# Optimization experiments

Hardware: AMD Instinct MI355X
Metric: run time of the kernel (lower is better)

Reference implementation:

```python
import jax, jax.numpy as jnp
import numpy as np

B, S, T = 512, 1024, 48  # batch, seq_len, num_tags


def setup_inputs() -> dict:
    key = jax.random.key(0)
    k1, k2, k3, k4, k5, k6 = jax.random.split(key, 6)
    emissions = jax.random.normal(k1, (B, S, T), dtype=jnp.float32)
    tags = jax.random.randint(k2, (B, S), 0, T)
    lengths = jax.random.randint(k3, (B,), 1, S + 1)
    mask = jnp.arange(S)[None, :] < lengths[:, None]  # contiguous prefix mask, bool
    # learned parameters (nn.Parameter zeros init in the module; use small random here)
    start_transitions = 0.01 * jax.random.normal(k4, (T,), dtype=jnp.float32)
    end_transitions = 0.01 * jax.random.normal(k5, (T,), dtype=jnp.float32)
    transitions = 0.01 * jax.random.normal(k6, (T, T), dtype=jnp.float32)
    return {
        "emissions": emissions,
        "tags": tags,
        "mask": mask,
        "start_transitions": start_transitions,
        "end_transitions": end_transitions,
        "transitions": transitions,
    }


def _log_partition(emissions, mask, start_transitions, end_transitions, transitions):
    # score[b, i] = log-sum over paths ending in tag i (note: this repo indexes
    # transitions[i, j] with j = previous tag inside the partition recursion).
    score0 = start_transitions[None, :] + emissions[:, 0]  # (B, T)

    def step(score, xs):
        emit_t, mask_t = xs  # (B, T), (B,)
        # score_t[b, i] = logsumexp_j(score[b, j] + transitions[i, j]) + emit_t[b, i]
        score_t = jax.nn.logsumexp(score[:, None, :] + transitions[None, :, :], axis=2) + emit_t
        score = jnp.where(mask_t[:, None], score_t, score)
        return score, None

    em = jnp.swapaxes(emissions[:, 1:], 0, 1)  # (S-1, B, T)
    mk = jnp.swapaxes(mask[:, 1:], 0, 1)       # (S-1, B)
    score, _ = jax.lax.scan(step, score0, (em, mk))
    return jax.nn.logsumexp(score + end_transitions[None, :], axis=1)  # (B,)


def _score_sentence(emissions, tags, mask, start_transitions, end_transitions, transitions):
    Bb = emissions.shape[0]
    bidx = jnp.arange(Bb)
    maskf = mask.astype(emissions.dtype)
    score = start_transitions[tags[:, 0]] + emissions[bidx, 0, tags[:, 0]]  # (B,)
    trans_sc = transitions[tags[:, :-1], tags[:, 1:]]  # (B, S-1)
    emit_sc = jnp.take_along_axis(emissions, tags[:, :, None], axis=2)[..., 0]  # (B, S)
    score = score + jnp.sum((trans_sc + emit_sc[:, 1:]) * maskf[:, 1:], axis=1)
    last_idx = jnp.sum(mask.astype(jnp.int32), axis=1) - 1  # (B,)
    last_tags = jnp.take_along_axis(tags, last_idx[:, None], axis=1)[:, 0]
    return score + end_transitions[last_tags]


def reference(emissions, tags, mask, start_transitions, end_transitions, transitions):
    log_denominator = _log_partition(emissions, mask, start_transitions, end_transitions, transitions)
    log_numerator = _score_sentence(emissions, tags, mask, start_transitions, end_transitions, transitions)
    return jnp.mean(log_denominator - log_numerator)
```

## Files before the change

kernel.cpp:

```cpp
#include <hip/hip_runtime.h>

#define BB 512
#define SS 1024
#define TT 48
#define GG 16
#define CK 8
#define NSLOT 5

typedef __attribute__((ext_vector_type(8))) short short8;
typedef __attribute__((ext_vector_type(4))) float float4v;
typedef unsigned uint2v __attribute__((ext_vector_type(2)));

__device__ __forceinline__ unsigned short f2bf(float x) {
    unsigned u = __float_as_uint(x);
    u += 0x7FFFu + ((u >> 16) & 1u);
    return (unsigned short)(u >> 16);
}
__device__ __forceinline__ unsigned pk2bf(float lo, float hi) {
#if __has_builtin(__builtin_amdgcn_cvt_pk_bf16_f32)
    typedef __bf16 bf16x2 __attribute__((ext_vector_type(2)));
    union { bf16x2 v; unsigned u; } cv;
    cv.v = __builtin_amdgcn_cvt_pk_bf16_f32(lo, hi);
    return cv.u;
#else
    return __builtin_amdgcn_perm(__float_as_uint(hi) + 0x8000u,
                                 __float_as_uint(lo) + 0x8000u, 0x07060302u);
#endif
}
__device__ __forceinline__ float bflo(unsigned u) { return __uint_as_float(u << 16); }
__device__ __forceinline__ float bfhi(unsigned u) { return __uint_as_float(u & 0xFFFF0000u); }
__device__ __forceinline__ float wave_sum(float v) {
#pragma unroll
    for (int off = 32; off >= 1; off >>= 1) v += __shfl_xor(v, off, 64);
    return v;
}
__device__ __forceinline__ int wave_sum_i(int v) {
#pragma unroll
    for (int off = 32; off >= 1; off >>= 1) v += __shfl_xor(v, off, 64);
    return v;
}
__device__ __forceinline__ float xgrp_max(float m) {
#if __has_builtin(__builtin_amdgcn_permlane16_swap) && __has_builtin(__builtin_amdgcn_permlane32_swap)
    uint2v a = __builtin_amdgcn_permlane16_swap(__float_as_uint(m), __float_as_uint(m), false, false);
    m = fmaxf(__uint_as_float(a[0]), __uint_as_float(a[1]));
    uint2v b = __builtin_amdgcn_permlane32_swap(__float_as_uint(m), __float_as_uint(m), false, false);
    m = fmaxf(__uint_as_float(b[0]), __uint_as_float(b[1]));
#else
    m = fmaxf(m, __shfl_xor(m, 16, 64));
    m = fmaxf(m, __shfl_xor(m, 32, 64));
#endif
    return m;
}
__device__ __forceinline__ float xgrp_sum(float m) {
#if __has_builtin(__builtin_amdgcn_permlane16_swap) && __has_builtin(__builtin_amdgcn_permlane32_swap)
    uint2v a = __builtin_amdgcn_permlane16_swap(__float_as_uint(m), __float_as_uint(m), false, false);
    m = __uint_as_float(a[0]) + __uint_as_float(a[1]);
    uint2v b = __builtin_amdgcn_permlane32_swap(__float_as_uint(m), __float_as_uint(m), false, false);
    m = __uint_as_float(b[0]) + __uint_as_float(b[1]);
#else
    m += __shfl_xor(m, 16, 64);
    m += __shfl_xor(m, 32, 64);
#endif
    return m;
}

__global__ __launch_bounds__(256)
void crf_numer(const float* __restrict__ em, const int* __restrict__ tags,
               const int* __restrict__ mask, const float* __restrict__ start_tr,
               const float* __restrict__ end_tr, const float* __restrict__ trans,
               float* __restrict__ numer, int* __restrict__ lenArr) {
    const int b = blockIdx.x, tid = threadIdx.x;
    const float* emb = em + (size_t)b * SS * TT;
    const int* tg = tags + (size_t)b * SS;
    const int* mk = mask + (size_t)b * SS;
    const int s0 = tid * 4;
    const int4 t4 = *(const int4*)(tg + s0);
    const int4 m4 = *(const int4*)(mk + s0);
    const int tprev = (tid == 0) ? 0 : tg[s0 - 1];
    int cnt = (m4.x != 0) + (m4.y != 0) + (m4.z != 0) + (m4.w != 0);
    float ns = 0.f;
    if (tid > 0 && m4.x) ns += trans[tprev * TT + t4.x] + emb[(size_t)s0 * TT + t4.x];
    if (m4.y) ns += trans[t4.x * TT + t4.y] + emb[(size_t)(s0 + 1) * TT + t4.y];
    if (m4.z) ns += trans[t4.y * TT + t4.z] + emb[(size_t)(s0 + 2) * TT + t4.z];
    if (m4.w) ns += trans[t4.z * TT + t4.w] + emb[(size_t)(s0 + 3) * TT + t4.w];
    float wsum = wave_sum(ns);
    int wcnt = wave_sum_i(cnt);
    __shared__ float sf[4]; __shared__ int si[4];
    if ((tid & 63) == 0) { sf[tid >> 6] = wsum; si[tid >> 6] = wcnt; }
    __syncthreads();
    if (tid == 0) {
        float tot = sf[0] + sf[1] + sf[2] + sf[3];
        int L = si[0] + si[1] + si[2] + si[3];
        int t0 = tg[0];
        tot += start_tr[t0] + emb[t0] + end_tr[tg[L - 1]];
        numer[b] = tot;
        lenArr[b] = L;
    }
}

__global__ __launch_bounds__(320, 1)
void crf_fwd(const float* __restrict__ em, const float* __restrict__ start_tr,
             const float* __restrict__ end_tr, const float* __restrict__ trans,
             const int* __restrict__ lenArr, float* __restrict__ denomArr) {
    __shared__ uint2 ring[NSLOT * CK * 3 * 64];

    const int tid = threadIdx.x;
    const int wave = tid >> 6, lane = tid & 63;
    const int wgbase = blockIdx.x * GG;

    if (wave == 0) {
        const int n = lane & 15, q = lane >> 4;
        const int bb = wgbase + n;

        short8 afr[3][2];
#pragma unroll
        for (int mt = 0; mt < 3; ++mt) {
            const int so = mt * 16 + n;
#pragma unroll
            for (int kt = 0; kt < 2; ++kt) {
                short8 a;
#pragma unroll
                for (int i = 0; i < 8; ++i) {
                    int si_;
                    if (kt == 0) si_ = (i < 4) ? (q * 4 + i) : (16 + q * 4 + (i - 4));
                    else         si_ = (i < 4) ? (32 + q * 4 + i) : -1;
                    a[i] = (si_ >= 0) ? (short)f2bf(__expf(trans[so * TT + si_])) : (short)0;
                }
                afr[mt][kt] = a;
            }
        }

        const float* em0 = em + (size_t)bb * SS * TT + q * 4;
        float p[3][4];
#pragma unroll
        for (int mt = 0; mt < 3; ++mt) {
            float4 v = *(const float4*)(em0 + mt * 16);
            int sb = mt * 16 + q * 4;
            p[mt][0] = __expf(start_tr[sb + 0] + v.x);
            p[mt][1] = __expf(start_tr[sb + 1] + v.y);
            p[mt][2] = __expf(start_tr[sb + 2] + v.z);
            p[mt][3] = __expf(start_tr[sb + 3] + v.w);
        }

        const int len = lenArr[bb];
        int Lmax = len;
#pragma unroll
        for (int off = 1; off < 64; off <<= 1) {
            int o = __shfl_xor(Lmax, off, 64);
            Lmax = Lmax > o ? Lmax : o;
        }
        const int P = (Lmax + 6) >> 3;

        bool cc0 = (len == 1);
        float dc[3][4];
#pragma unroll
        for (int mt = 0; mt < 3; ++mt)
#pragma unroll
            for (int r = 0; r < 4; ++r) dc[mt][r] = cc0 ? p[mt][r] : 0.f;
        float lcap = 0.f, logscale = 0.f;
        const float4v Z = {0.f, 0.f, 0.f, 0.f};

        for (int pp = -3; pp < P; ++pp) {
            if (pp >= 0) {
                const uint2* rp = &ring[(pp % NSLOT) * (CK * 3 * 64) + lane];
                uint2 emch[8][3];
#pragma unroll
                for (int u = 0; u < 8; ++u) {
#pragma unroll
                    for (int j = 0; j < 3; ++j)
                        emch[u][j] = rp[u * 192 + j * 64];
                }
                const int lo = 8 * pp + 2, hi = 8 * pp + 9;
                const bool any = __ballot((len >= lo) & (len <= hi)) != 0ull;
#pragma unroll
                for (int u = 0; u < 8; ++u) {
                    union { short8 v; unsigned w[4]; } B0, B1;
                    B0.w[0] = pk2bf(p[0][0], p[0][1]); B0.w[1] = pk2bf(p[0][2], p[0][3]);
                    B0.w[2] = pk2bf(p[1][0], p[1][1]); B0.w[3] = pk2bf(p[1][2], p[1][3]);
                    B1.w[0] = pk2bf(p[2][0], p[2][1]); B1.w[1] = pk2bf(p[2][2], p[2][3]);
                    B1.w[2] = 0u; B1.w[3] = 0u;
                    float4v A0 = __builtin_amdgcn_mfma_f32_16x16x32_bf16(afr[0][0], B0.v, Z, 0, 0, 0);
                    float4v A1 = __builtin_amdgcn_mfma_f32_16x16x32_bf16(afr[1][0], B0.v, Z, 0, 0, 0);
                    float4v A2 = __builtin_amdgcn_mfma_f32_16x16x32_bf16(afr[2][0], B0.v, Z, 0, 0, 0);
                    A0 = __builtin_amdgcn_mfma_f32_16x16x32_bf16(afr[0][1], B1.v, A0, 0, 0, 0);
                    A1 = __builtin_amdgcn_mfma_f32_16x16x32_bf16(afr[1][1], B1.v, A1, 0, 0, 0);
                    A2 = __builtin_amdgcn_mfma_f32_16x16x32_bf16(afr[2][1], B1.v, A2, 0, 0, 0);
                    const uint2 c0 = emch[u][0], c1 = emch[u][1], c2v = emch[u][2];
                    p[0][0] = A0[0] * bflo(c0.x); p[0][1] = A0[1] * bfhi(c0.x);
                    p[0][2] = A0[2] * bflo(c0.y); p[0][3] = A0[3] * bfhi(c0.y);
                    p[1][0] = A1[0] * bflo(c1.x); p[1][1] = A1[1] * bfhi(c1.x);
                    p[1][2] = A1[2] * bflo(c1.y); p[1][3] = A1[3] * bfhi(c1.y);
                    p[2][0] = A2[0] * bflo(c2v.x); p[2][1] = A2[1] * bfhi(c2v.x);
                    p[2][2] = A2[2] * bflo(c2v.y); p[2][3] = A2[3] * bfhi(c2v.y);
                    if (any) {
                        bool cc = (len == 8 * pp + u + 2);
#pragma unroll
                        for (int mt = 0; mt < 3; ++mt)
#pragma unroll
                            for (int r = 0; r < 4; ++r) dc[mt][r] = cc ? p[mt][r] : dc[mt][r];
                        lcap = cc ? logscale : lcap;
                    }
                    if (u == 7) {
                        float m = fmaxf(fmaxf(p[0][0], p[0][1]), fmaxf(p[0][2], p[0][3]));
                        m = fmaxf(m, fmaxf(fmaxf(p[1][0], p[1][1]), fmaxf(p[1][2], p[1][3])));
                        m = fmaxf(m, fmaxf(fmaxf(p[2][0], p[2][1]), fmaxf(p[2][2], p[2][3])));
                        m = fmaxf(xgrp_max(m), 1e-30f);
                        logscale += __logf(m);
                        float rm = __builtin_amdgcn_rcpf(m);
#pragma unroll
                        for (int mt = 0; mt < 3; ++mt)
#pragma unroll
                            for (int r = 0; r < 4; ++r) p[mt][r] *= rm;
                    }
                }
            }
            __builtin_amdgcn_s_barrier();
        }

        float pe = 0.f;
#pragma unroll
        for (int mt = 0; mt < 3; ++mt) {
            int sb = mt * 16 + q * 4;
            pe = fmaf(dc[mt][0], __expf(end_tr[sb + 0]), pe);
            pe = fmaf(dc[mt][1], __expf(end_tr[sb + 1]), pe);
            pe = fmaf(dc[mt][2], __expf(end_tr[sb + 2]), pe);
            pe = fmaf(dc[mt][3], __expf(end_tr[sb + 3]), pe);
        }
        pe = xgrp_sum(pe);
        if (lane < 16) denomArr[bb] = lcap + __logf(pe);

    } else {
        const int T = (wave - 1) >> 1;
        const int sub = (wave - 1) & 1;
        const int nb = lane & 15, q4 = lane >> 4;
        const int bb = wgbase + nb;
        const int len_v = lenArr[bb];
        int Lmax = len_v;
#pragma unroll
        for (int off = 1; off < 64; off <<= 1) {
            int o = __shfl_xor(Lmax, off, 64);
            Lmax = Lmax > o ? Lmax : o;
        }
        const int P = (Lmax + 6) >> 3;

        const float* emP = em + (size_t)bb * SS * TT + q4 * 4;
        float4 buf[12];

        for (int pp = -3; pp < P; ++pp) {
            int cv = pp + 1;
            if (cv >= 0 && cv < P && (cv & 1) == T) {
                uint2* wp = &ring[(cv % NSLOT) * (CK * 3 * 64) + lane];
#pragma unroll
                for (int k = 0; k < 12; ++k) {
                    const int i = sub * 12 + k, u = i / 3, j = i % 3;
                    int t = 1 + 8 * cv + u;
                    bool live = t < len_v;
                    float4 v = buf[k];
                    unsigned ox = pk2bf(__expf(v.x), __expf(v.y));
                    unsigned oy = pk2bf(__expf(v.z), __expf(v.w));
                    uint2 o;
                    o.x = live ? ox : 0u;
                    o.y = live ? oy : 0u;
                    wp[u * 192 + j * 64] = o;
                }
            }
            int ci = pp + 3;
            if (ci < P && (ci & 1) == T) {
#pragma unroll
                for (int k = 0; k < 12; ++k) {
                    const int i = sub * 12 + k, u = i / 3, j = i % 3;
                    int t = 1 + 8 * ci + u; t = t < SS ? t : SS - 1;
                    buf[k] = *(const float4*)(emP + (size_t)t * TT + j * 16);
                }
            }
            __builtin_amdgcn_s_waitcnt(0xC07F);
            __builtin_amdgcn_s_barrier();
        }
    }
}

__global__ __launch_bounds__(64)
void crf_reduce(const float* __restrict__ denom, const float* __restrict__ numer,
                float* __restrict__ out) {
    int lane = threadIdx.x;
    float s = 0.f;
    for (int i = lane; i < BB; i += 64) s += denom[i] - numer[i];
    s = wave_sum(s);
    if (lane == 0) out[0] = s * (1.0f / (float)BB);
}

extern "C" void kernel_launch(void* const* d_in, const int* in_sizes, int n_in,
                              void* d_out, int out_size, void* d_ws, size_t ws_size,
                              hipStream_t stream) {
    const float* emissions = (const float*)d_in[0];
    const int*   tags      = (const int*)d_in[1];
    const int*   mask      = (const int*)d_in[2];
    const float* start_tr  = (const float*)d_in[3];
    const float* end_tr    = (const float*)d_in[4];
    const float* trans     = (const float*)d_in[5];

    char* ws = (char*)d_ws;
    float* denom = (float*)ws;
    float* numer = (float*)(ws + 2048);
    int*   lenA  = (int*)(ws + 4096);

    crf_numer<<<BB, 256, 0, stream>>>(emissions, tags, mask, start_tr, end_tr,
                                      trans, numer, lenA);
    crf_fwd<<<BB / GG, 320, 0, stream>>>(emissions, start_tr, end_tr, trans,
                                         lenA, denom);
    crf_reduce<<<1, 64, 0, stream>>>(denom, numer, (float*)d_out);
}
```

Measured before the change: 324.5 us.

## Stage fp32 exp-emissions in LDS and software-prefetch per step in scan wave

The producer waves now write fp32 exp(emission) values into the shared ring instead of packed bf16, and the ring depth is cut from five to four slots to fit the larger entries in LDS. The MFMA scan wave no longer bulk-loads all eight steps of a chunk into registers. It loads the next step's three vectors while the current step's MFMAs run, which lowers register pressure and removes the bf16 unpack work. The scan wave also raises its scheduling priority with s_setprio. The costs are double the LDS traffic and footprint per chunk, and one less slot of producer slack.

```diff
diff --git a/kernel.cpp b/kernel.cpp
--- a/kernel.cpp
+++ b/kernel.cpp
@@ -5,7 +5,7 @@
 #define TT 48
 #define GG 16
 #define CK 8
-#define NSLOT 5
+#define NSLOT 4
 
 typedef __attribute__((ext_vector_type(8))) short short8;
 typedef __attribute__((ext_vector_type(4))) float float4v;
@@ -27,8 +27,6 @@
                                  __float_as_uint(lo) + 0x8000u, 0x07060302u);
 #endif
 }
-__device__ __forceinline__ float bflo(unsigned u) { return __uint_as_float(u << 16); }
-__device__ __forceinline__ float bfhi(unsigned u) { return __uint_as_float(u & 0xFFFF0000u); }
 __device__ __forceinline__ float wave_sum(float v) {
 #pragma unroll
     for (int off = 32; off >= 1; off >>= 1) v += __shfl_xor(v, off, 64);
@@ -102,13 +100,15 @@
 void crf_fwd(const float* __restrict__ em, const float* __restrict__ start_tr,
              const float* __restrict__ end_tr, const float* __restrict__ trans,
              const int* __restrict__ lenArr, float* __restrict__ denomArr) {
-    __shared__ uint2 ring[NSLOT * CK * 3 * 64];
+    __shared__ float4v ring[NSLOT * CK * 3 * 64];
 
     const int tid = threadIdx.x;
     const int wave = tid >> 6, lane = tid & 63;
     const int wgbase = blockIdx.x * GG;
+    const float4v Zv = {0.f, 0.f, 0.f, 0.f};
 
     if (wave == 0) {
+        __builtin_amdgcn_s_setprio(1);
         const int n = lane & 15, q = lane >> 4;
         const int bb = wgbase + n;
 
@@ -131,15 +131,18 @@
         }
 
         const float* em0 = em + (size_t)bb * SS * TT + q * 4;
-        float p[3][4];
-#pragma unroll
-        for (int mt = 0; mt < 3; ++mt) {
-            float4 v = *(const float4*)(em0 + mt * 16);
-            int sb = mt * 16 + q * 4;
-            p[mt][0] = __expf(start_tr[sb + 0] + v.x);
-            p[mt][1] = __expf(start_tr[sb + 1] + v.y);
-            p[mt][2] = __expf(start_tr[sb + 2] + v.z);
-            p[mt][3] = __expf(start_tr[sb + 3] + v.w);
+        float4v p0, p1, p2;
+        {
+            float4v v0 = *(const float4v*)(em0);
+            float4v v1 = *(const float4v*)(em0 + 16);
+            float4v v2 = *(const float4v*)(em0 + 32);
+            const int sb = q * 4;
+#pragma unroll
+            for (int r = 0; r < 4; ++r) {
+                p0[r] = __expf(start_tr[sb + r] + v0[r]);
+                p1[r] = __expf(start_tr[16 + sb + r] + v1[r]);
+                p2[r] = __expf(start_tr[32 + sb + r] + v2[r]);
+            }
         }
 
         const int len = lenArr[bb];
@@ -151,66 +154,50 @@
         }
         const int P = (Lmax + 6) >> 3;
 
-        bool cc0 = (len == 1);
-        float dc[3][4];
-#pragma unroll
-        for (int mt = 0; mt < 3; ++mt)
-#pragma unroll
-            for (int r = 0; r < 4; ++r) dc[mt][r] = cc0 ? p[mt][r] : 0.f;
+        const bool cc0 = (len == 1);
+        float4v dc0 = cc0 ? p0 : Zv, dc1 = cc0 ? p1 : Zv, dc2 = cc0 ? p2 : Zv;
         float lcap = 0.f, logscale = 0.f;
-        const float4v Z = {0.f, 0.f, 0.f, 0.f};
 
         for (int pp = -3; pp < P; ++pp) {
             if (pp >= 0) {
-                const uint2* rp = &ring[(pp % NSLOT) * (CK * 3 * 64) + lane];
-                uint2 emch[8][3];
-#pragma unroll
-                for (int u = 0; u < 8; ++u) {
-#pragma unroll
-                    for (int j = 0; j < 3; ++j)
-                        emch[u][j] = rp[u * 192 + j * 64];
-                }
+                const float4v* rp = ring + (size_t)(pp % NSLOT) * (CK * 3 * 64) + lane;
+                float4v e0 = rp[0], e1 = rp[64], e2 = rp[128];
                 const int lo = 8 * pp + 2, hi = 8 * pp + 9;
                 const bool any = __ballot((len >= lo) & (len <= hi)) != 0ull;
 #pragma unroll
                 for (int u = 0; u < 8; ++u) {
                     union { short8 v; unsigned w[4]; } B0, B1;
-                    B0.w[0] = pk2bf(p[0][0], p[0][1]); B0.w[1] = pk2bf(p[0][2], p[0][3]);
-                    B0.w[2] = pk2bf(p[1][0], p[1][1]); B0.w[3] = pk2bf(p[1][2], p[1][3]);
-                    B1.w[0] = pk2bf(p[2][0], p[2][1]); B1.w[1] = pk2bf(p[2][2], p[2][3]);
+                    B0.w[0] = pk2bf(p0[0], p0[1]); B0.w[1] = pk2bf(p0[2], p0[3]);
+                    B0.w[2] = pk2bf(p1[0], p1[1]); B0.w[3] = pk2bf(p1[2], p1[3]);
+                    B1.w[0] = pk2bf(p2[0], p2[1]); B1.w[1] = pk2bf(p2[2], p2[3]);
                     B1.w[2] = 0u; B1.w[3] = 0u;
-                    float4v A0 = __builtin_amdgcn_mfma_f32_16x16x32_bf16(afr[0][0], B0.v, Z, 0, 0, 0);
-                    float4v A1 = __builtin_amdgcn_mfma_f32_16x16x32_bf16(afr[1][0], B0.v, Z, 0, 0, 0);
-                    float4v A2 = __builtin_amdgcn_mfma_f32_16x16x32_bf16(afr[2][0], B0.v, Z, 0, 0, 0);
+                    float4v A0 = __builtin_amdgcn_mfma_f32_16x16x32_bf16(afr[0][0], B0.v, Zv, 0, 0, 0);
+                    float4v A1 = __builtin_amdgcn_mfma_f32_16x16x32_bf16(afr[1][0], B0.v, Zv, 0, 0, 0);
+                    float4v A2 = __builtin_amdgcn_mfma_f32_16x16x32_bf16(afr[2][0], B0.v, Zv, 0, 0, 0);
                     A0 = __builtin_amdgcn_mfma_f32_16x16x32_bf16(afr[0][1], B1.v, A0, 0, 0, 0);
                     A1 = __builtin_amdgcn_mfma_f32_16x16x32_bf16(afr[1][1], B1.v, A1, 0, 0, 0);
                     A2 = __builtin_amdgcn_mfma_f32_16x16x32_bf16(afr[2][1], B1.v, A2, 0, 0, 0);
-                    const uint2 c0 = emch[u][0], c1 = emch[u][1], c2v = emch[u][2];
-                    p[0][0] = A0[0] * bflo(c0.x); p[0][1] = A0[1] * bfhi(c0.x);
-                    p[0][2] = A0[2] * bflo(c0.y); p[0][3] = A0[3] * bfhi(c0.y);
-                    p[1][0] = A1[0] * bflo(c1.x); p[1][1] = A1[1] * bfhi(c1.x);
-                    p[1][2] = A1[2] * bflo(c1.y); p[1][3] = A1[3] * bfhi(c1.y);
-                    p[2][0] = A2[0] * bflo(c2v.x); p[2][1] = A2[1] * bfhi(c2v.x);
-                    p[2][2] = A2[2] * bflo(c2v.y); p[2][3] = A2[3] * bfhi(c2v.y);
+                    float4v n0, n1, n2;
+                    if (u < 7) {
+                        n0 = rp[(u + 1) * 192];
+                        n1 = rp[(u + 1) * 192 + 64];
+                        n2 = rp[(u + 1) * 192 + 128];
+                    }
+                    p0 = A0 * e0; p1 = A1 * e1; p2 = A2 * e2;
                     if (any) {
-                        bool cc = (len == 8 * pp + u + 2);
-#pragma unroll
-                        for (int mt = 0; mt < 3; ++mt)
-#pragma unroll
-                            for (int r = 0; r < 4; ++r) dc[mt][r] = cc ? p[mt][r] : dc[mt][r];
+                        const bool cc = (len == 8 * pp + u + 2);
+                        dc0 = cc ? p0 : dc0; dc1 = cc ? p1 : dc1; dc2 = cc ? p2 : dc2;
                         lcap = cc ? logscale : lcap;
                     }
+                    e0 = n0; e1 = n1; e2 = n2;
                     if (u == 7) {
-                        float m = fmaxf(fmaxf(p[0][0], p[0][1]), fmaxf(p[0][2], p[0][3]));
-                        m = fmaxf(m, fmaxf(fmaxf(p[1][0], p[1][1]), fmaxf(p[1][2], p[1][3])));
-                        m = fmaxf(m, fmaxf(fmaxf(p[2][0], p[2][1]), fmaxf(p[2][2], p[2][3])));
+                        float m = fmaxf(fmaxf(p0[0], p0[1]), fmaxf(p0[2], p0[3]));
+                        m = fmaxf(m, fmaxf(fmaxf(p1[0], p1[1]), fmaxf(p1[2], p1[3])));
+                        m = fmaxf(m, fmaxf(fmaxf(p2[0], p2[1]), fmaxf(p2[2], p2[3])));
                         m = fmaxf(xgrp_max(m), 1e-30f);
                         logscale += __logf(m);
-                        float rm = __builtin_amdgcn_rcpf(m);
-#pragma unroll
-                        for (int mt = 0; mt < 3; ++mt)
-#pragma unroll
-                            for (int r = 0; r < 4; ++r) p[mt][r] *= rm;
+                        const float rm = __builtin_amdgcn_rcpf(m);
+                        p0 *= rm; p1 *= rm; p2 *= rm;
                     }
                 }
             }
@@ -218,13 +205,14 @@
         }
 
         float pe = 0.f;
-#pragma unroll
-        for (int mt = 0; mt < 3; ++mt) {
-            int sb = mt * 16 + q * 4;
-            pe = fmaf(dc[mt][0], __expf(end_tr[sb + 0]), pe);
-            pe = fmaf(dc[mt][1], __expf(end_tr[sb + 1]), pe);
-            pe = fmaf(dc[mt][2], __expf(end_tr[sb + 2]), pe);
-            pe = fmaf(dc[mt][3], __expf(end_tr[sb + 3]), pe);
+        {
+            const int sb = q * 4;
+#pragma unroll
+            for (int r = 0; r < 4; ++r) {
+                pe = fmaf(dc0[r], __expf(end_tr[sb + r]), pe);
+                pe = fmaf(dc1[r], __expf(end_tr[16 + sb + r]), pe);
+                pe = fmaf(dc2[r], __expf(end_tr[32 + sb + r]), pe);
+            }
         }
         pe = xgrp_sum(pe);
         if (lane < 16) denomArr[bb] = lcap + __logf(pe);
@@ -245,23 +233,23 @@
 
         const float* emP = em + (size_t)bb * SS * TT + q4 * 4;
         float4 buf[12];
+        const float4v Z4 = {0.f, 0.f, 0.f, 0.f};
 
         for (int pp = -3; pp < P; ++pp) {
             int cv = pp + 1;
             if (cv >= 0 && cv < P && (cv & 1) == T) {
-                uint2* wp = &ring[(cv % NSLOT) * (CK * 3 * 64) + lane];
+                float4v* wp = ring + (size_t)(cv % NSLOT) * (CK * 3 * 64) + lane;
 #pragma unroll
                 for (int k = 0; k < 12; ++k) {
                     const int i = sub * 12 + k, u = i / 3, j = i % 3;
-                    int t = 1 + 8 * cv + u;
-                    bool live = t < len_v;
+                    const int t = 1 + 8 * cv + u;
+                    const bool live = t < len_v;
                     float4 v = buf[k];
-                    unsigned ox = pk2bf(__expf(v.x), __expf(v.y));
-                    unsigned oy = pk2bf(__expf(v.z), __expf(v.w));
-                    uint2 o;
-                    o.x = live ? ox : 0u;
-                    o.y = live ? oy : 0u;
-                    wp[u * 192 + j * 64] = o;
+                    float4v o;
+                    o[0] = __expf(v.x); o[1] = __expf(v.y);
+                    o[2] = __expf(v.z); o[3] = __expf(v.w);
+                    o = live ? o : Z4;
+                    wp[(size_t)(u * 3 + j) * 64] = o;
                 }
             }
             int ci = pp + 3;
```

Measured after the change: 299.3 us. 1.08x faster.
